# Kernel tuning notes

Measured on AMD Instinct MI355X. Metric: run time of the kernel, lower is better.

Reference implementation:

```python
import jax, jax.numpy as jnp
import numpy as np

H = 501
T = 200
V = 71


def gru_layer(x, h0, W_ih, W_hh, b_ih, b_hh):
    # x: [B,T,I], h0: [B,H]; PyTorch GRU gate order: r, z, n
    gi = jnp.einsum('bti,gi->btg', x, W_ih) + b_ih  # [B,T,3H]

    def step(h, gi_t):
        gh = h @ W_hh.T + b_hh  # [B,3H]
        r = jax.nn.sigmoid(gi_t[:, :H] + gh[:, :H])
        z = jax.nn.sigmoid(gi_t[:, H:2 * H] + gh[:, H:2 * H])
        n = jnp.tanh(gi_t[:, 2 * H:] + r * gh[:, 2 * H:])
        h_new = (1.0 - z) * n + z * h
        return h_new, h_new

    h_last, ys = jax.lax.scan(step, h0, jnp.swapaxes(gi, 0, 1))
    return jnp.swapaxes(ys, 0, 1), h_last  # [B,T,H], [B,H]


def setup_inputs() -> dict:
    key = jax.random.key(0)
    ks = jax.random.split(key, 16)
    s = 1.0 / np.sqrt(H)
    u = lambda k, shp: jax.random.uniform(k, shp, jnp.float32, -s, s)
    return {
        'x': jax.random.normal(ks[0], (256, 1), jnp.float32),
        'W_ih1': u(ks[1], (3 * H, 1)), 'W_hh1': u(ks[2], (3 * H, H)),
        'b_ih1': u(ks[3], (3 * H,)), 'b_hh1': u(ks[4], (3 * H,)),
        'W_ih2': u(ks[5], (3 * H, H)), 'W_hh2': u(ks[6], (3 * H, H)),
        'b_ih2': u(ks[7], (3 * H,)), 'b_hh2': u(ks[8], (3 * H,)),
        'W_ih3': u(ks[9], (3 * H, H)), 'W_hh3': u(ks[10], (3 * H, H)),
        'b_ih3': u(ks[11], (3 * H,)), 'b_hh3': u(ks[12], (3 * H,)),
        'Wd': u(ks[13], (V, H)), 'bd': u(ks[14], (V,)),
    }


def reference(x, W_ih1, W_hh1, b_ih1, b_hh1, W_ih2, W_hh2, b_ih2, b_hh2,
              W_ih3, W_hh3, b_ih3, b_hh3, Wd, bd):
    B = x.shape[0]
    # repeat_vector: tile latent scalar across T timesteps -> [B,T,1]
    xr = jnp.broadcast_to(x[:, None, :], (B, T, 1))
    h0 = jnp.zeros((B, H), x.dtype)
    o1, h1 = gru_layer(xr, h0, W_ih1, W_hh1, b_ih1, b_hh1)
    o1 = jnp.tanh(o1)
    o2, h2 = gru_layer(o1, h1, W_ih2, W_hh2, b_ih2, b_hh2)
    o2 = jnp.tanh(o2)
    o3, _ = gru_layer(o2, h2, W_ih3, W_hh3, b_ih3, b_hh3)
    o3 = jnp.tanh(o3)
    logits = jax.nn.relu(jnp.einsum('bth,vh->btv', o3, Wd) + bd)  # [B,T,V]
    return logits
```

## Files before the change

### kernel.cpp

```cpp
#include <hip/hip_runtime.h>
#include <hip/hip_fp16.h>

typedef _Float16 half8 __attribute__((ext_vector_type(8)));
typedef float floatx16 __attribute__((ext_vector_type(16)));

#define HID 501
#define TT  200
#define BB  256
#define VV  71
#define HP  512

#define OFF_BAR   0ull
#define OFF_HFRAG 4096ull
#define SZ_HFRAG  (2ull*8*32*512*2)
#define OFF_HFIN  (OFF_HFRAG + SZ_HFRAG)
#define SZ_HFIN   (256ull*512*4)
#define OFF_GI1   (OFF_HFIN + SZ_HFIN)
#define SZ_GI1    (256ull*1536*4)
#define OFF_BIAS  (OFF_GI1 + SZ_GI1)
#define SZ_BIAS   (65536ull)
#define OFF_WD    (OFF_BIAS + SZ_BIAS)
#define SZ_WD     (96ull*512*2)
#define OFF_BD    (OFF_WD + SZ_WD)
#define SZ_BD     4096ull
#define OFF_W     (OFF_BD + SZ_BD)
#define SZ_W      (3ull*2*32*2*32*1024*2)
#define OFF_OFRAG (OFF_W + SZ_W)
#define SZ_OBUF   (8ull*200*32*512*2)
#define WS_NEED   (OFF_OFRAG + 2ull*SZ_OBUF)

#define COH_LD16(dst, p) \
  asm volatile("global_load_dwordx4 %0, %1, off sc0 sc1" : "=&v"(dst) : "v"(p) : "memory")

__device__ __forceinline__ void coh_store16(_Float16* p, half8 v) {
  asm volatile("global_store_dwordx4 %0, %1, off sc0 sc1" :: "v"(p), "v"(v) : "memory");
}
__device__ __forceinline__ unsigned coh_ld4(const unsigned* p) {
  unsigned v;
  asm volatile("global_load_dword %0, %1, off sc0 sc1\n\ts_waitcnt vmcnt(0)"
               : "=&v"(v) : "v"(p) : "memory");
  return v;
}
__device__ __forceinline__ void coh_st4(unsigned* p, unsigned v) {
  asm volatile("global_store_dword %0, %1, off sc0 sc1" :: "v"(p), "v"(v) : "memory");
}
__device__ __forceinline__ float tanh_fast(float x) {
  float e = __expf(2.f*x);
  return 1.f - 2.f/(e + 1.f);
}

__global__ __launch_bounds__(256) void prep_weights(
    const float* __restrict__ wih1, const float* __restrict__ whh1,
    const float* __restrict__ wih2, const float* __restrict__ whh2,
    const float* __restrict__ wih3, const float* __restrict__ whh3,
    _Float16* __restrict__ wbuf)
{
  const float* WIH[3] = {wih1, wih2, wih3};
  const float* WHH[3] = {whh1, whh2, whh3};
  const long total = 3ll << 21;
  for (long idx = (long)blockIdx.x*256 + threadIdx.x; idx < total; idx += (long)gridDim.x*256) {
    int k   = (int)(idx & 1023);
    int row = (int)((idx >> 10) & 31);
    int rt  = (int)((idx >> 15) & 1);
    int blk = (int)((idx >> 16) & 31);
    int L   = (int)(idx >> 21);
    int g, hl; bool ok;
    if (rt == 0) { g = row >> 4; hl = row & 15; ok = true; }
    else         { g = 2;        hl = row & 15; ok = (row < 16); }
    int hcol = blk*16 + hl;
    ok = ok && (hcol < HID);
    float w = 0.f;
    if (ok) {
      if (k < HP) { if (L > 0 && k < HID) w = WIH[L][(g*HID + hcol)*HID + k]; }
      else        { int kk = k - HP; if (kk < HID) w = WHH[L][(g*HID + hcol)*HID + kk]; }
    }
    _Float16 wh = (_Float16)w;
    _Float16 wl = (_Float16)(w - (float)wh);
    long oh = ((((long)(L*2+0)*32 + blk)*2 + rt)*32 + row)*1024 + k;
    long ol = ((((long)(L*2+1)*32 + blk)*2 + rt)*32 + row)*1024 + k;
    wbuf[oh] = wh;
    wbuf[ol] = wl;
  }
}

__global__ __launch_bounds__(256) void prep_misc(
    const float* __restrict__ x, const float* __restrict__ wih1,
    const float* __restrict__ bih1, const float* __restrict__ bhh1,
    const float* __restrict__ bih2, const float* __restrict__ bhh2,
    const float* __restrict__ bih3, const float* __restrict__ bhh3,
    const float* __restrict__ wd, const float* __restrict__ bd,
    float* __restrict__ gi1, float* __restrict__ bias,
    _Float16* __restrict__ wdbuf, float* __restrict__ bdbuf)
{
  const int N1 = 256*1536;
  const int N2 = 3*2*1536;
  const int N3 = 96*512;
  const int N4 = 96;
  for (int idx = blockIdx.x*256 + threadIdx.x; idx < N1+N2+N3+N4; idx += gridDim.x*256) {
    if (idx < N1) {
      int b = idx / 1536, m = idx % 1536;
      int g = m >> 9, hc = m & 511;
      float v = 0.f;
      if (hc < HID) { int r = g*HID + hc; v = x[b]*wih1[r] + bih1[r]; }
      gi1[idx] = v;
    } else if (idx < N1+N2) {
      int i2 = idx - N1;
      int L = i2 / (2*1536);
      int rest = i2 % (2*1536);
      int pl = rest / 1536, m = rest % 1536;
      int g = m >> 9, hc = m & 511;
      float v = 0.f;
      if (hc < HID) {
        int r = g*HID + hc;
        if (pl == 0) v = (L==0) ? 0.f : (L==1 ? bih2[r] : bih3[r]);
        else         v = (L==0) ? bhh1[r] : (L==1 ? bhh2[r] : bhh3[r]);
      }
      bias[i2] = v;
    } else if (idx < N1+N2+N3) {
      int i3 = idx - (N1+N2);
      int v = i3 >> 9, k = i3 & 511;
      float val = (v < VV && k < HID) ? wd[v*HID + k] : 0.f;
      wdbuf[i3] = (_Float16)val;
    } else {
      int v = idx - (N1+N2+N3);
      bdbuf[v] = (v < VV) ? bd[v] : 0.f;
    }
  }
}

template<int L>
__global__ __launch_bounds__(512, 2) void gru_layer_k(
    const _Float16* __restrict__ wbuf,
    const _Float16* __restrict__ osrc,
    _Float16* __restrict__ odst,
    _Float16* __restrict__ hfrag,
    float* __restrict__ hfin,
    const float* __restrict__ gi1,
    const float* __restrict__ bias,
    unsigned* __restrict__ flags)
{
  constexpr int KPW = (L==0) ? 4 : 8;
  const int bid  = blockIdx.x;
  const int tile = bid & 7;
  const int sl   = bid >> 3;
  const int tid  = threadIdx.x;
  const int w    = tid >> 6;
  const int lane = tid & 63;

  __shared__ float    ldsC[8][2][32][32];
  __shared__ _Float16 ldsH[2][32][16];

  half8 Wf[2][2][KPW];
  {
    int row = lane & 31;
    int kc  = (lane >> 5) << 3;
    int ks0 = (L==0) ? (32 + w*4) : (w*8);
    #pragma unroll
    for (int pl = 0; pl < 2; ++pl)
      #pragma unroll
      for (int rt = 0; rt < 2; ++rt)
        #pragma unroll
        for (int i = 0; i < KPW; ++i) {
          long off = ((((long)(L*2+pl)*32 + sl)*2 + rt)*32 + row)*1024 + (long)(ks0+i)*16 + kc;
          Wf[pl][rt][i] = *(const half8*)(wbuf + off);
        }
  }

  const int b     = tid & 31;
  const int hl    = (tid >> 5) & 15;
  const int bglob = tile*32 + b;
  const int hglob = sl*16 + hl;
  float hreg = 0.f;
  float bih[3], bhh[3], gi[3] = {0,0,0};
  if (L > 0) hreg = hfin[bglob*HP + hglob];
  #pragma unroll
  for (int g = 0; g < 3; ++g) {
    bih[g] = bias[(L*2+0)*1536 + g*512 + hglob];
    bhh[g] = bias[(L*2+1)*1536 + g*512 + hglob];
    if (L == 0) gi[g] = gi1[(long)bglob*1536 + g*512 + hglob];
  }

  const long hf_par  = 8ll*32*512;
  const long hf_tile = (long)tile*(32*512);
  const long ob_t    = (long)tile*200*(32*512);
  const long region  = (long)sl*512;
  unsigned* fl = flags + tile*32;
  unsigned dead = 0;

  for (int t = 0; t < TT; ++t) {
    if (L > 0 && w < 4) {
      const _Float16* xb = osrc + ob_t + (long)t*(32*512) + (long)(w*8)*512 + lane*8;
      half8 X[8];
      #pragma unroll
      for (int i = 0; i < 8; ++i) X[i] = *(const half8*)(xb + i*512);
      floatx16 C0, C1;
      #pragma unroll
      for (int i = 0; i < 16; ++i) { C0[i] = 0.f; C1[i] = 0.f; }
      #pragma unroll
      for (int i = 0; i < 8; ++i) {
        C0 = __builtin_amdgcn_mfma_f32_32x32x16_f16(Wf[0][0][i], X[i], C0, 0, 0, 0);
        C0 = __builtin_amdgcn_mfma_f32_32x32x16_f16(Wf[1][0][i], X[i], C0, 0, 0, 0);
        C1 = __builtin_amdgcn_mfma_f32_32x32x16_f16(Wf[0][1][i], X[i], C1, 0, 0, 0);
        C1 = __builtin_amdgcn_mfma_f32_32x32x16_f16(Wf[1][1][i], X[i], C1, 0, 0, 0);
      }
      int col = lane & 31, rb = (lane >> 5) << 2;
      #pragma unroll
      for (int r = 0; r < 16; ++r) {
        int rowm = (r & 3) + 8*(r >> 2) + rb;
        ldsC[w][0][rowm][col] = C0[r];
        ldsC[w][1][rowm][col] = C1[r];
      }
    }
    if (t > 0) {
      if (w == 0 && !dead) {
        const unsigned tgt = (unsigned)(L*(TT-1) + t);
        const unsigned* fp = fl + (lane & 31);
        unsigned tries = 0;
        for (;;) {
          unsigned v = coh_ld4(fp);
          if (__all(v >= tgt)) break;
          if (++tries > (1u<<18)) { dead = 1; break; }
        }
      }
      __syncthreads();
    }
    if ((L == 0 || w >= 4) && !(L == 0 && t == 0)) {
      const int hs0 = (L==0) ? (w*4) : ((w-4)*8);
      const _Float16* hp = hfrag + (long)(t & 1)*hf_par + hf_tile + (long)hs0*512 + lane*8;
      half8 H[KPW];
      #pragma unroll
      for (int i = 0; i < KPW; ++i) COH_LD16(H[i], hp + i*512);
      asm volatile("s_waitcnt vmcnt(0)" ::: "memory");
      __builtin_amdgcn_sched_barrier(0);
      floatx16 C0, C1;
      #pragma unroll
      for (int i = 0; i < 16; ++i) { C0[i] = 0.f; C1[i] = 0.f; }
      #pragma unroll
      for (int i = 0; i < KPW; ++i) {
        C0 = __builtin_amdgcn_mfma_f32_32x32x16_f16(Wf[0][0][i], H[i], C0, 0, 0, 0);
        C0 = __builtin_amdgcn_mfma_f32_32x32x16_f16(Wf[1][0][i], H[i], C0, 0, 0, 0);
        C1 = __builtin_amdgcn_mfma_f32_32x32x16_f16(Wf[0][1][i], H[i], C1, 0, 0, 0);
        C1 = __builtin_amdgcn_mfma_f32_32x32x16_f16(Wf[1][1][i], H[i], C1, 0, 0, 0);
      }
      int col = lane & 31, rb = (lane >> 5) << 2;
      #pragma unroll
      for (int r = 0; r < 16; ++r) {
        int rowm = (r & 3) + 8*(r >> 2) + rb;
        ldsC[w][0][rowm][col] = C0[r];
        ldsC[w][1][rowm][col] = C1[r];
      }
    }
    __syncthreads();
    {
      float sx[3] = {0,0,0}, sh[3] = {0,0,0};
      if (!(L == 0 && t == 0)) {
        #pragma unroll
        for (int g = 0; g < 3; ++g) {
          int rt  = (g == 2) ? 1 : 0;
          int row = (g == 2) ? hl : g*16 + hl;
          float ax = 0.f, ah = 0.f;
          if (L == 0) {
            #pragma unroll
            for (int ww = 0; ww < 8; ++ww) ah += ldsC[ww][rt][row][b];
          } else {
            #pragma unroll
            for (int ww = 0; ww < 4; ++ww) ax += ldsC[ww][rt][row][b];
            #pragma unroll
            for (int ww = 4; ww < 8; ++ww) ah += ldsC[ww][rt][row][b];
          }
          sx[g] = ax; sh[g] = ah;
        }
      }
      float pr = sx[0] + gi[0] + bih[0] + sh[0] + bhh[0];
      float pz = sx[1] + gi[1] + bih[1] + sh[1] + bhh[1];
      float r = 1.f/(1.f + __expf(-pr));
      float z = 1.f/(1.f + __expf(-pz));
      float n = tanh_fast(sx[2] + gi[2] + bih[2] + r*(sh[2] + bhh[2]));
      float hn = (1.f - z)*n + z*hreg;
      hreg = hn;
      ldsH[0][b][hl] = (_Float16)hn;
      ldsH[1][b][hl] = (_Float16)tanh_fast(hn);
      if (t == TT-1) hfin[bglob*HP + hglob] = hn;
    }
    __syncthreads();
    if (tid < 64) {
      int h0 = (tid >> 5) * 8;
      half8 hv = *(const half8*)&ldsH[0][tid & 31][h0];
      half8 ov = *(const half8*)&ldsH[1][tid & 31][h0];
      *(half8*)(odst + ob_t + (long)t*(32*512) + region + tid*8) = ov;
      coh_store16(hfrag + (long)((t+1) & 1)*hf_par + hf_tile + region + tid*8, hv);
    }
    if (w == 0) {
      asm volatile("s_waitcnt vmcnt(0)" ::: "memory");
      if (tid == 0 && t < TT-1)
        coh_st4(fl + sl, (unsigned)(L*(TT-1) + t + 1));
    }
  }
}

__global__ __launch_bounds__(256, 2) void decoder_k(
    const _Float16* __restrict__ o3,
    const _Float16* __restrict__ wdbuf,
    const float* __restrict__ bdbuf,
    float* __restrict__ out)
{
  const int bx = blockIdx.x;
  const int tile = bx & 7;
  const int chunk = bx >> 3;
  const int tid = threadIdx.x;
  const int w = tid >> 6, lane = tid & 63;
  __shared__ float ldsD[4][96][32];
  __shared__ float ldsO[32][73];

  half8 Wf[3][8];
  {
    int kc = (lane >> 5) << 3;
    #pragma unroll
    for (int mt = 0; mt < 3; ++mt)
      #pragma unroll
      for (int i = 0; i < 8; ++i) {
        int row = mt*32 + (lane & 31);
        int k = (w*8 + i)*16 + kc;
        Wf[mt][i] = *(const half8*)(wdbuf + (long)row*512 + k);
      }
  }
  for (int tt = 0; tt < 8; ++tt) {
    int t = chunk*8 + tt;
    long ob = ((long)tile*200 + t)*(32*512);
    half8 Xf[8];
    #pragma unroll
    for (int i = 0; i < 8; ++i) {
      int s = w*8 + i;
      Xf[i] = *(const half8*)(o3 + ob + (long)s*512 + lane*8);
    }
    floatx16 C0, C1, C2;
    #pragma unroll
    for (int i = 0; i < 16; ++i) { C0[i] = 0.f; C1[i] = 0.f; C2[i] = 0.f; }
    #pragma unroll
    for (int i = 0; i < 8; ++i) {
      C0 = __builtin_amdgcn_mfma_f32_32x32x16_f16(Wf[0][i], Xf[i], C0, 0, 0, 0);
      C1 = __builtin_amdgcn_mfma_f32_32x32x16_f16(Wf[1][i], Xf[i], C1, 0, 0, 0);
      C2 = __builtin_amdgcn_mfma_f32_32x32x16_f16(Wf[2][i], Xf[i], C2, 0, 0, 0);
    }
    {
      int col = lane & 31;
      int rb = (lane >> 5) << 2;
      #pragma unroll
      for (int r = 0; r < 16; ++r) {
        int rowm = (r & 3) + 8*(r >> 2) + rb;
        ldsD[w][rowm][col]      = C0[r];
        ldsD[w][32 + rowm][col] = C1[r];
        ldsD[w][64 + rowm][col] = C2[r];
      }
    }
    __syncthreads();
    for (int ii = tid; ii < VV*32; ii += 256) {
      int bb = ii & 31, v = ii >> 5;
      float s = ldsD[0][v][bb] + ldsD[1][v][bb] + ldsD[2][v][bb] + ldsD[3][v][bb] + bdbuf[v];
      ldsO[bb][v] = s > 0.f ? s : 0.f;
    }
    __syncthreads();
    for (int ii = tid; ii < VV*32; ii += 256) {
      int bb = ii / VV, v = ii - bb*VV;
      out[((long)(tile*32 + bb)*200 + t)*VV + v] = ldsO[bb][v];
    }
    __syncthreads();
  }
}

extern "C" void kernel_launch(void* const* d_in, const int* in_sizes, int n_in,
                              void* d_out, int out_size, void* d_ws, size_t ws_size,
                              hipStream_t stream) {
  (void)in_sizes; (void)n_in;
  const float* x    = (const float*)d_in[0];
  const float* wih1 = (const float*)d_in[1];
  const float* whh1 = (const float*)d_in[2];
  const float* bih1 = (const float*)d_in[3];
  const float* bhh1 = (const float*)d_in[4];
  const float* wih2 = (const float*)d_in[5];
  const float* whh2 = (const float*)d_in[6];
  const float* bih2 = (const float*)d_in[7];
  const float* bhh2 = (const float*)d_in[8];
  const float* wih3 = (const float*)d_in[9];
  const float* whh3 = (const float*)d_in[10];
  const float* bih3 = (const float*)d_in[11];
  const float* bhh3 = (const float*)d_in[12];
  const float* wd   = (const float*)d_in[13];
  const float* bd   = (const float*)d_in[14];
  char* ws = (char*)d_ws;

  if (ws_size < WS_NEED) {
    hipMemsetAsync(d_out, 0, (size_t)out_size*sizeof(float), stream);
    return;
  }

  _Float16* wbuf   = (_Float16*)(ws + OFF_W);
  float*    gi1p   = (float*)(ws + OFF_GI1);
  float*    biasp  = (float*)(ws + OFF_BIAS);
  _Float16* wdbufp = (_Float16*)(ws + OFF_WD);
  float*    bdbufp = (float*)(ws + OFF_BD);
  _Float16* hfragp = (_Float16*)(ws + OFF_HFRAG);
  float*    hfinp  = (float*)(ws + OFF_HFIN);
  unsigned* flagsp = (unsigned*)(ws + OFF_BAR);
  _Float16* ob0    = (_Float16*)(ws + OFF_OFRAG);
  _Float16* ob1    = ob0 + SZ_OBUF/2;

  hipMemsetAsync(ws + OFF_BAR, 0, 4096, stream);

  prep_weights<<<4096, 256, 0, stream>>>(wih1, whh1, wih2, whh2, wih3, whh3, wbuf);
  prep_misc<<<1024, 256, 0, stream>>>(x, wih1, bih1, bhh1, bih2, bhh2, bih3, bhh3,
                                      wd, bd, gi1p, biasp, wdbufp, bdbufp);

  gru_layer_k<0><<<256, 512, 0, stream>>>(wbuf, ob1, ob0, hfragp, hfinp, gi1p, biasp, flagsp);
  gru_layer_k<1><<<256, 512, 0, stream>>>(wbuf, ob0, ob1, hfragp, hfinp, gi1p, biasp, flagsp);
  gru_layer_k<2><<<256, 512, 0, stream>>>(wbuf, ob1, ob0, hfragp, hfinp, gi1p, biasp, flagsp);

  decoder_k<<<200, 256, 0, stream>>>(ob0, wdbufp, bdbufp, (float*)d_out);
}
```

Baseline: 2.174 ms.

## Interleave two batch tiles per block in GRU layers 2 and 3

The layer kernel gains an NPH template parameter. For layers 2 and 3 each block now handles two batch tiles in alternating phases, so the grid drops from 256 to 128 blocks while each block keeps its per-slice weights in registers. The idea is that while one tile waits on its cross-block flag, the other tile's work can fill the gap, and fewer blocks take part in each flag barrier. The hidden-state fragment store and flag release now happen before the activation output store, to shorten the recurrent critical path. The cost is twice the serial work per block per timestep and more syncthreads per step. The spin timeout is also raised.

```diff
diff --git a/kernel.cpp b/kernel.cpp
--- a/kernel.cpp
+++ b/kernel.cpp
@@ -31,7 +31,6 @@
 
 #define COH_LD16(dst, p) \
   asm volatile("global_load_dwordx4 %0, %1, off sc0 sc1" : "=&v"(dst) : "v"(p) : "memory")
-
 __device__ __forceinline__ void coh_store16(_Float16* p, half8 v) {
   asm volatile("global_store_dwordx4 %0, %1, off sc0 sc1" :: "v"(p), "v"(v) : "memory");
 }
@@ -128,7 +127,7 @@
   }
 }
 
-template<int L>
+template<int L, int NPH>
 __global__ __launch_bounds__(512, 2) void gru_layer_k(
     const _Float16* __restrict__ wbuf,
     const _Float16* __restrict__ osrc,
@@ -141,11 +140,13 @@
 {
   constexpr int KPW = (L==0) ? 4 : 8;
   const int bid  = blockIdx.x;
-  const int tile = bid & 7;
-  const int sl   = bid >> 3;
   const int tid  = threadIdx.x;
   const int w    = tid >> 6;
   const int lane = tid & 63;
+
+  int tiles[NPH], sl;
+  if (NPH == 1) { tiles[0] = bid & 7; sl = bid >> 3; }
+  else          { tiles[0] = bid & 3; tiles[1] = (bid & 3) + 4; sl = bid >> 2; }
 
   __shared__ float    ldsC[8][2][32][32];
   __shared__ _Float16 ldsH[2][32][16];
@@ -168,132 +169,146 @@
 
   const int b     = tid & 31;
   const int hl    = (tid >> 5) & 15;
-  const int bglob = tile*32 + b;
   const int hglob = sl*16 + hl;
-  float hreg = 0.f;
-  float bih[3], bhh[3], gi[3] = {0,0,0};
-  if (L > 0) hreg = hfin[bglob*HP + hglob];
+  float bih[3], bhh[3];
   #pragma unroll
   for (int g = 0; g < 3; ++g) {
     bih[g] = bias[(L*2+0)*1536 + g*512 + hglob];
     bhh[g] = bias[(L*2+1)*1536 + g*512 + hglob];
-    if (L == 0) gi[g] = gi1[(long)bglob*1536 + g*512 + hglob];
-  }
-
-  const long hf_par  = 8ll*32*512;
-  const long hf_tile = (long)tile*(32*512);
-  const long ob_t    = (long)tile*200*(32*512);
-  const long region  = (long)sl*512;
-  unsigned* fl = flags + tile*32;
+  }
+  int       bglob[NPH];
+  float     hreg[NPH];
+  float     gi[NPH][3];
+  long      ob_t[NPH], hf_t[NPH];
+  unsigned* fl[NPH];
+  #pragma unroll
+  for (int ph = 0; ph < NPH; ++ph) {
+    bglob[ph] = tiles[ph]*32 + b;
+    hreg[ph]  = (L > 0) ? hfin[bglob[ph]*HP + hglob] : 0.f;
+    #pragma unroll
+    for (int g = 0; g < 3; ++g)
+      gi[ph][g] = (L == 0) ? gi1[(long)bglob[ph]*1536 + g*512 + hglob] : 0.f;
+    ob_t[ph] = (long)tiles[ph]*200*(32*512);
+    hf_t[ph] = (long)tiles[ph]*(32*512);
+    fl[ph]   = flags + tiles[ph]*32;
+  }
+  const long hf_par = 8ll*32*512;
+  const long region = (long)sl*512;
   unsigned dead = 0;
 
   for (int t = 0; t < TT; ++t) {
-    if (L > 0 && w < 4) {
-      const _Float16* xb = osrc + ob_t + (long)t*(32*512) + (long)(w*8)*512 + lane*8;
-      half8 X[8];
-      #pragma unroll
-      for (int i = 0; i < 8; ++i) X[i] = *(const half8*)(xb + i*512);
-      floatx16 C0, C1;
-      #pragma unroll
-      for (int i = 0; i < 16; ++i) { C0[i] = 0.f; C1[i] = 0.f; }
-      #pragma unroll
-      for (int i = 0; i < 8; ++i) {
-        C0 = __builtin_amdgcn_mfma_f32_32x32x16_f16(Wf[0][0][i], X[i], C0, 0, 0, 0);
-        C0 = __builtin_amdgcn_mfma_f32_32x32x16_f16(Wf[1][0][i], X[i], C0, 0, 0, 0);
-        C1 = __builtin_amdgcn_mfma_f32_32x32x16_f16(Wf[0][1][i], X[i], C1, 0, 0, 0);
-        C1 = __builtin_amdgcn_mfma_f32_32x32x16_f16(Wf[1][1][i], X[i], C1, 0, 0, 0);
-      }
-      int col = lane & 31, rb = (lane >> 5) << 2;
-      #pragma unroll
-      for (int r = 0; r < 16; ++r) {
-        int rowm = (r & 3) + 8*(r >> 2) + rb;
-        ldsC[w][0][rowm][col] = C0[r];
-        ldsC[w][1][rowm][col] = C1[r];
-      }
-    }
-    if (t > 0) {
-      if (w == 0 && !dead) {
-        const unsigned tgt = (unsigned)(L*(TT-1) + t);
-        const unsigned* fp = fl + (lane & 31);
-        unsigned tries = 0;
-        for (;;) {
-          unsigned v = coh_ld4(fp);
-          if (__all(v >= tgt)) break;
-          if (++tries > (1u<<18)) { dead = 1; break; }
+    #pragma unroll
+    for (int ph = 0; ph < NPH; ++ph) {
+      if (L > 0 && w < 4) {
+        const _Float16* xb = osrc + ob_t[ph] + (long)t*(32*512) + (long)(w*8)*512 + lane*8;
+        half8 X[8];
+        #pragma unroll
+        for (int i = 0; i < 8; ++i) X[i] = *(const half8*)(xb + i*512);
+        floatx16 C0, C1;
+        #pragma unroll
+        for (int i = 0; i < 16; ++i) { C0[i] = 0.f; C1[i] = 0.f; }
+        #pragma unroll
+        for (int i = 0; i < 8; ++i) {
+          C0 = __builtin_amdgcn_mfma_f32_32x32x16_f16(Wf[0][0][i], X[i], C0, 0, 0, 0);
+          C0 = __builtin_amdgcn_mfma_f32_32x32x16_f16(Wf[1][0][i], X[i], C0, 0, 0, 0);
+          C1 = __builtin_amdgcn_mfma_f32_32x32x16_f16(Wf[0][1][i], X[i], C1, 0, 0, 0);
+          C1 = __builtin_amdgcn_mfma_f32_32x32x16_f16(Wf[1][1][i], X[i], C1, 0, 0, 0);
+        }
+        int col = lane & 31, rb = (lane >> 5) << 2;
+        #pragma unroll
+        for (int r = 0; r < 16; ++r) {
+          int rowm = (r & 3) + 8*(r >> 2) + rb;
+          ldsC[w][0][rowm][col] = C0[r];
+          ldsC[w][1][rowm][col] = C1[r];
+        }
+      }
+      if (t > 0) {
+        if (w == 0 && !dead) {
+          const unsigned tgt = (unsigned)(L*(TT-1) + t);
+          const unsigned* fp = fl[ph] + (lane & 31);
+          unsigned tries = 0;
+          for (;;) {
+            unsigned v = coh_ld4(fp);
+            if (__all(v >= tgt)) break;
+            if (++tries > (1u<<19)) { dead = 1; break; }
+          }
+        }
+        __syncthreads();
+      }
+      if ((L == 0 || w >= 4) && !(L == 0 && t == 0)) {
+        const int hs0 = (L==0) ? (w*4) : ((w-4)*8);
+        const _Float16* hp = hfrag + (long)(t & 1)*hf_par + hf_t[ph] + (long)hs0*512 + lane*8;
+        half8 H[KPW];
+        #pragma unroll
+        for (int i = 0; i < KPW; ++i) COH_LD16(H[i], hp + i*512);
+        asm volatile("s_waitcnt vmcnt(0)" ::: "memory");
+        __builtin_amdgcn_sched_barrier(0);
+        floatx16 C0, C1;
+        #pragma unroll
+        for (int i = 0; i < 16; ++i) { C0[i] = 0.f; C1[i] = 0.f; }
+        #pragma unroll
+        for (int i = 0; i < KPW; ++i) {
+          C0 = __builtin_amdgcn_mfma_f32_32x32x16_f16(Wf[0][0][i], H[i], C0, 0, 0, 0);
+          C0 = __builtin_amdgcn_mfma_f32_32x32x16_f16(Wf[1][0][i], H[i], C0, 0, 0, 0);
+          C1 = __builtin_amdgcn_mfma_f32_32x32x16_f16(Wf[0][1][i], H[i], C1, 0, 0, 0);
+          C1 = __builtin_amdgcn_mfma_f32_32x32x16_f16(Wf[1][1][i], H[i], C1, 0, 0, 0);
+        }
+        int col = lane & 31, rb = (lane >> 5) << 2;
+        #pragma unroll
+        for (int r = 0; r < 16; ++r) {
+          int rowm = (r & 3) + 8*(r >> 2) + rb;
+          ldsC[w][0][rowm][col] = C0[r];
+          ldsC[w][1][rowm][col] = C1[r];
         }
       }
       __syncthreads();
-    }
-    if ((L == 0 || w >= 4) && !(L == 0 && t == 0)) {
-      const int hs0 = (L==0) ? (w*4) : ((w-4)*8);
-      const _Float16* hp = hfrag + (long)(t & 1)*hf_par + hf_tile + (long)hs0*512 + lane*8;
-      half8 H[KPW];
-      #pragma unroll
-      for (int i = 0; i < KPW; ++i) COH_LD16(H[i], hp + i*512);
-      asm volatile("s_waitcnt vmcnt(0)" ::: "memory");
-      __builtin_amdgcn_sched_barrier(0);
-      floatx16 C0, C1;
-      #pragma unroll
-      for (int i = 0; i < 16; ++i) { C0[i] = 0.f; C1[i] = 0.f; }
-      #pragma unroll
-      for (int i = 0; i < KPW; ++i) {
-        C0 = __builtin_amdgcn_mfma_f32_32x32x16_f16(Wf[0][0][i], H[i], C0, 0, 0, 0);
-        C0 = __builtin_amdgcn_mfma_f32_32x32x16_f16(Wf[1][0][i], H[i], C0, 0, 0, 0);
-        C1 = __builtin_amdgcn_mfma_f32_32x32x16_f16(Wf[0][1][i], H[i], C1, 0, 0, 0);
-        C1 = __builtin_amdgcn_mfma_f32_32x32x16_f16(Wf[1][1][i], H[i], C1, 0, 0, 0);
-      }
-      int col = lane & 31, rb = (lane >> 5) << 2;
-      #pragma unroll
-      for (int r = 0; r < 16; ++r) {
-        int rowm = (r & 3) + 8*(r >> 2) + rb;
-        ldsC[w][0][rowm][col] = C0[r];
-        ldsC[w][1][rowm][col] = C1[r];
-      }
-    }
-    __syncthreads();
-    {
-      float sx[3] = {0,0,0}, sh[3] = {0,0,0};
-      if (!(L == 0 && t == 0)) {
-        #pragma unroll
-        for (int g = 0; g < 3; ++g) {
-          int rt  = (g == 2) ? 1 : 0;
-          int row = (g == 2) ? hl : g*16 + hl;
-          float ax = 0.f, ah = 0.f;
-          if (L == 0) {
-            #pragma unroll
-            for (int ww = 0; ww < 8; ++ww) ah += ldsC[ww][rt][row][b];
-          } else {
-            #pragma unroll
-            for (int ww = 0; ww < 4; ++ww) ax += ldsC[ww][rt][row][b];
-            #pragma unroll
-            for (int ww = 4; ww < 8; ++ww) ah += ldsC[ww][rt][row][b];
+      {
+        float sx[3] = {0,0,0}, sh[3] = {0,0,0};
+        if (!(L == 0 && t == 0)) {
+          #pragma unroll
+          for (int g = 0; g < 3; ++g) {
+            int rt  = (g == 2) ? 1 : 0;
+            int row = (g == 2) ? hl : g*16 + hl;
+            float ax = 0.f, ah = 0.f;
+            if (L == 0) {
+              #pragma unroll
+              for (int ww = 0; ww < 8; ++ww) ah += ldsC[ww][rt][row][b];
+            } else {
+              #pragma unroll
+              for (int ww = 0; ww < 4; ++ww) ax += ldsC[ww][rt][row][b];
+              #pragma unroll
+              for (int ww = 4; ww < 8; ++ww) ah += ldsC[ww][rt][row][b];
+            }
+            sx[g] = ax; sh[g] = ah;
           }
-          sx[g] = ax; sh[g] = ah;
-        }
-      }
-      float pr = sx[0] + gi[0] + bih[0] + sh[0] + bhh[0];
-      float pz = sx[1] + gi[1] + bih[1] + sh[1] + bhh[1];
-      float r = 1.f/(1.f + __expf(-pr));
-      float z = 1.f/(1.f + __expf(-pz));
-      float n = tanh_fast(sx[2] + gi[2] + bih[2] + r*(sh[2] + bhh[2]));
-      float hn = (1.f - z)*n + z*hreg;
-      hreg = hn;
-      ldsH[0][b][hl] = (_Float16)hn;
-      ldsH[1][b][hl] = (_Float16)tanh_fast(hn);
-      if (t == TT-1) hfin[bglob*HP + hglob] = hn;
-    }
-    __syncthreads();
-    if (tid < 64) {
-      int h0 = (tid >> 5) * 8;
-      half8 hv = *(const half8*)&ldsH[0][tid & 31][h0];
-      half8 ov = *(const half8*)&ldsH[1][tid & 31][h0];
-      *(half8*)(odst + ob_t + (long)t*(32*512) + region + tid*8) = ov;
-      coh_store16(hfrag + (long)((t+1) & 1)*hf_par + hf_tile + region + tid*8, hv);
-    }
-    if (w == 0) {
-      asm volatile("s_waitcnt vmcnt(0)" ::: "memory");
-      if (tid == 0 && t < TT-1)
-        coh_st4(fl + sl, (unsigned)(L*(TT-1) + t + 1));
+        }
+        float pr = sx[0] + gi[ph][0] + bih[0] + sh[0] + bhh[0];
+        float pz = sx[1] + gi[ph][1] + bih[1] + sh[1] + bhh[1];
+        float r = 1.f/(1.f + __expf(-pr));
+        float z = 1.f/(1.f + __expf(-pz));
+        float n = tanh_fast(sx[2] + gi[ph][2] + bih[2] + r*(sh[2] + bhh[2]));
+        float hn = (1.f - z)*n + z*hreg[ph];
+        hreg[ph] = hn;
+        ldsH[0][b][hl] = (_Float16)hn;
+        ldsH[1][b][hl] = (_Float16)tanh_fast(hn);
+        if (t == TT-1) hfin[bglob[ph]*HP + hglob] = hn;
+      }
+      __syncthreads();
+      if (tid < 64) {
+        int h0 = (tid >> 5) * 8;
+        half8 hv = *(const half8*)&ldsH[0][tid & 31][h0];
+        coh_store16(hfrag + (long)((t+1) & 1)*hf_par + hf_t[ph] + region + tid*8, hv);
+      }
+      if (w == 0) {
+        asm volatile("s_waitcnt vmcnt(0)" ::: "memory");
+        if (tid == 0 && t < TT-1)
+          coh_st4(fl[ph] + sl, (unsigned)(L*(TT-1) + t + 1));
+      }
+      if (tid < 64) {
+        int h0 = (tid >> 5) * 8;
+        half8 ov = *(const half8*)&ldsH[1][tid & 31][h0];
+        *(half8*)(odst + ob_t[ph] + (long)t*(32*512) + region + tid*8) = ov;
+      }
     }
   }
 }
@@ -411,9 +426,9 @@
   prep_misc<<<1024, 256, 0, stream>>>(x, wih1, bih1, bhh1, bih2, bhh2, bih3, bhh3,
                                       wd, bd, gi1p, biasp, wdbufp, bdbufp);
 
-  gru_layer_k<0><<<256, 512, 0, stream>>>(wbuf, ob1, ob0, hfragp, hfinp, gi1p, biasp, flagsp);
-  gru_layer_k<1><<<256, 512, 0, stream>>>(wbuf, ob0, ob1, hfragp, hfinp, gi1p, biasp, flagsp);
-  gru_layer_k<2><<<256, 512, 0, stream>>>(wbuf, ob1, ob0, hfragp, hfinp, gi1p, biasp, flagsp);
+  gru_layer_k<0,1><<<256, 512, 0, stream>>>(wbuf, ob1, ob0, hfragp, hfinp, gi1p, biasp, flagsp);
+  gru_layer_k<1,2><<<128, 512, 0, stream>>>(wbuf, ob0, ob1, hfragp, hfinp, gi1p, biasp, flagsp);
+  gru_layer_k<2,2><<<128, 512, 0, stream>>>(wbuf, ob1, ob0, hfragp, hfinp, gi1p, biasp, flagsp);
 
   decoder_k<<<200, 256, 0, stream>>>(ob0, wdbufp, bdbufp, (float*)d_out);
 }
```

After: 3.796 ms. 1.75x slower.
